# Optimization experiments

Measured on AMD Instinct MI355X. Metric: run time of the kernel, lower is better.

## Reference

```python
import jax, jax.numpy as jnp
import numpy as np
import math

B, H, D, P, N = 65536, 256, 32, 16, 32768
LOG_C = math.log(math.sqrt(2.0 * math.pi))


def setup_inputs() -> dict:
    key = jax.random.key(0)
    ks = jax.random.split(key, 8)
    h = jax.random.normal(ks[0], (B, H), dtype=jnp.float32)
    p = jax.random.normal(ks[1], (B, 2 * D), dtype=jnp.float32)
    X_obs = jax.random.normal(ks[2], (N, D), dtype=jnp.float32)
    M_obs = (jax.random.uniform(ks[3], (N, D)) < 0.5).astype(jnp.float32)
    i_obs = jnp.arange(N, dtype=jnp.int32)  # unique indices into batch rows
    std = math.sqrt(2.0 / (4 + P))
    w_prep = std * jax.random.normal(ks[4], (D, 4, P), dtype=jnp.float32)
    bias_prep = 0.1 * jnp.ones((D, P), dtype=jnp.float32)
    # keras GRUCell params (reset_after=True): kernel [in,3H], recurrent [H,3H], two biases [3H]
    gru_kernel = 0.05 * jax.random.normal(ks[5], (P * D, 3 * H), dtype=jnp.float32)
    gru_rec_kernel = 0.05 * jax.random.normal(ks[6], (H, 3 * H), dtype=jnp.float32)
    gru_bias_in = jnp.zeros((3 * H,), dtype=jnp.float32)
    gru_bias_rec = jnp.zeros((3 * H,), dtype=jnp.float32)
    return {"h": h, "p": p, "X_obs": X_obs, "M_obs": M_obs, "i_obs": i_obs,
            "w_prep": w_prep, "bias_prep": bias_prep,
            "gru_kernel": gru_kernel, "gru_rec_kernel": gru_rec_kernel,
            "gru_bias_in": gru_bias_in, "gru_bias_rec": gru_bias_rec}


def _gru_cell(x, h_prev, kernel, rec_kernel, bias_in, bias_rec):
    # keras GRUCell, reset_after=True, tanh / sigmoid activations
    mx = x @ kernel + bias_in            # [N, 3H]
    mh = h_prev @ rec_kernel + bias_rec  # [N, 3H]
    xz, xr, xh = jnp.split(mx, 3, axis=1)
    rz, rr, rh = jnp.split(mh, 3, axis=1)
    z = jax.nn.sigmoid(xz + rz)
    r = jax.nn.sigmoid(xr + rr)
    hh = jnp.tanh(xh + r * rh)
    return z * h_prev + (1.0 - z) * hh


def reference(h, p, X_obs, M_obs, i_obs, w_prep, bias_prep,
              gru_kernel, gru_rec_kernel, gru_bias_in, gru_bias_rec):
    d, ph = w_prep.shape[0], w_prep.shape[2]
    p_obs = p[i_obs]                      # gather [N, 2D]
    mean, logvar = jnp.split(p_obs, 2, axis=1)
    sigma = jnp.exp(0.5 * logvar)
    error = (X_obs - mean) / sigma
    losses = 0.5 * ((error * error + logvar + 2.0 * LOG_C) * M_obs)  # [N, D]
    gi = jnp.stack([X_obs, mean, logvar, error], axis=2)             # [N, D, 4]
    gi = jnp.einsum('ndk,dkp->ndp', gi, w_prep) + bias_prep          # per-feature matmul
    gi = jax.nn.relu(gi)
    gi = jnp.transpose(gi, (2, 0, 1))                                # [P, N, D]
    gi = (gi * M_obs).reshape(-1, ph * d)                            # [N, P*D] (TF reshape semantics)
    h_obs = h[i_obs]
    h_new = _gru_cell(gi, h_obs, gru_kernel, gru_rec_kernel, gru_bias_in, gru_bias_rec)
    h_out = h.at[i_obs].set(h_new)                                   # scatter-update
    return (h_out, losses)
```

## Files before the change

### kernel.cpp

```cpp
#include <hip/hip_runtime.h>
#include <hip/hip_bf16.h>
#include <math.h>

#define NROWS 32768
#define DD 32
#define PPH 16
#define HH 256
#define BB 65536
#define TWO_LOG_C 1.8378770664093453f

typedef __attribute__((ext_vector_type(8))) __bf16 bf16x8;
typedef __attribute__((ext_vector_type(4))) float f32x4;
typedef unsigned int u32;

__device__ __forceinline__ float sigm_f(float x) { return 1.0f / (1.0f + __expf(-x)); }
__device__ __forceinline__ float tanh_f(float x) { return 1.0f - 2.0f / (1.0f + __expf(2.0f * x)); }

__device__ __forceinline__ void gl_lds16(const __bf16* g, __bf16* l) {
    __builtin_amdgcn_global_load_lds(
        (const __attribute__((address_space(1))) u32*)g,
        (__attribute__((address_space(3))) u32*)l, 16, 0, 0);
}

__global__ __launch_bounds__(256) void prep_kernel(
    const float* __restrict__ p,
    const float* __restrict__ X_obs,
    const float* __restrict__ M_obs,
    const int*   __restrict__ i_obs,
    const float* __restrict__ w_prep,
    const float* __restrict__ bias_prep,
    float* __restrict__ losses_out,
    __bf16* __restrict__ G)
{
    __shared__ float w2[64][33];
    __shared__ float b2[16][33];
    int tid = threadIdx.x;
    for (int i = tid; i < 2048; i += 256) w2[i & 63][i >> 6] = w_prep[i];
    for (int i = tid; i < 512; i += 256)  b2[i & 15][i >> 4] = bias_prep[i];
    __syncthreads();

    int gid = blockIdx.x * 256 + tid;
    int n = gid >> 5;
    int d = gid & 31;
    int idx = i_obs[n];

    float mean   = p[idx * (2 * DD) + d];
    float logvar = p[idx * (2 * DD) + DD + d];
    float x      = X_obs[gid];
    float m      = M_obs[gid];

    float inv_sigma = __expf(-0.5f * logvar);
    float err = (x - mean) * inv_sigma;
    losses_out[gid] = 0.5f * ((err * err + logvar + TWO_LOG_C) * m);

    #pragma unroll
    for (int q = 0; q < PPH; ++q) {
        float v = x      * w2[q][d]
                + mean   * w2[16 + q][d]
                + logvar * w2[32 + q][d]
                + err    * w2[48 + q][d]
                + b2[q][d];
        v = fmaxf(v, 0.0f) * m;
        G[(size_t)q * (NROWS * DD) + gid] = (__bf16)v;
    }
}

__global__ __launch_bounds__(256) void mask_zero_kernel(u32* __restrict__ mask32) {
    mask32[blockIdx.x * 256 + threadIdx.x] = 0;
}
__global__ __launch_bounds__(256) void mask_set_kernel(
    const int* __restrict__ i_obs, unsigned char* __restrict__ mask) {
    mask[i_obs[blockIdx.x * 256 + threadIdx.x]] = 1;
}
__global__ __launch_bounds__(256) void copy_h_masked_kernel(
    const float4* __restrict__ h, const unsigned char* __restrict__ mask,
    float4* __restrict__ out, int n4)
{
    int i = blockIdx.x * 256 + threadIdx.x;
    int stride = gridDim.x * 256;
    for (; i < n4; i += stride) {
        int row = i >> 6;
        if (!mask[row]) out[i] = h[i];
    }
}

__global__ __launch_bounds__(256) void hgather_kernel(
    const float* __restrict__ h, const int* __restrict__ i_obs,
    __bf16* __restrict__ Hb)
{
    int gid = blockIdx.x * 256 + threadIdx.x;
    int n = gid >> 5, c = gid & 31;
    const float* src = h + (size_t)i_obs[n] * 256 + c * 8;
    float4 a = ((const float4*)src)[0];
    float4 b = ((const float4*)src)[1];
    bf16x8 v;
    v[0] = (__bf16)a.x; v[1] = (__bf16)a.y; v[2] = (__bf16)a.z; v[3] = (__bf16)a.w;
    v[4] = (__bf16)b.x; v[5] = (__bf16)b.y; v[6] = (__bf16)b.z; v[7] = (__bf16)b.w;
    *(bf16x8*)(Hb + (size_t)n * 256 + c * 8) = v;
}

__global__ __launch_bounds__(256) void transpose_w_kernel(
    const float* __restrict__ src, __bf16* __restrict__ dst, int K)
{
    __shared__ float t[64][65];
    int k0 = blockIdx.x * 64;
    int j0 = blockIdx.y * 64;
    int tx = threadIdx.x & 63, ty = threadIdx.x >> 6;
    #pragma unroll
    for (int i = 0; i < 16; ++i) {
        int k = ty * 16 + i;
        t[k][tx] = src[(size_t)(k0 + k) * 768 + j0 + tx];
    }
    __syncthreads();
    #pragma unroll
    for (int i = 0; i < 16; ++i) {
        int j = ty * 16 + i;
        dst[(size_t)(j0 + j) * K + k0 + tx] = (__bf16)t[tx][j];
    }
}

#define A_EL 4096
#define B_EL 6144

struct StageCtx {
    const __bf16 *G, *Hb, *Kt, *Rt;
    int i0, j0, wave, lane;
};

__device__ __forceinline__ void stage_step(int t, const StageCtx& c,
                                           __bf16* ldsA, __bf16* ldsB) {
    const bool ph1 = t < 16;
    const int k0 = (ph1 ? t : (t - 16)) * 32;
    const int Kd = ph1 ? 512 : 256;
    const __bf16* Asrc = ph1 ? c.G : c.Hb;
    const __bf16* Bsrc = ph1 ? c.Kt : c.Rt;
    __bf16* dA = ldsA + (t & 1) * A_EL;
    __bf16* dB = ldsB + (t & 1) * B_EL;
    #pragma unroll
    for (int s = 0; s < 5; ++s) {
        int u = c.wave * 5 + s;
        if (u < 8) {
            int sA = u * 64 + c.lane;
            int kg = sA >> 7, row = sA & 127;
            gl_lds16(Asrc + (size_t)(c.i0 + row) * Kd + k0 + kg * 8,
                     dA + u * 64 * 8);
        } else {
            int sB = (u - 8) * 64 + c.lane;
            int mat = sB >> 8, w = sB & 255;
            int bkg = w >> 6, bj = w & 63;
            gl_lds16(Bsrc + (size_t)(mat * 256 + c.j0 + bj) * Kd + k0 + bkg * 8,
                     dB + (u - 8) * 64 * 8);
        }
    }
}

__device__ __forceinline__ void compute_step(
    const __bf16* cA, const __bf16* cB,
    int kgrp, int lrow, int rw, int cw,
    f32x4 (&az)[4][2], f32x4 (&ar)[4][2], f32x4 (&ah)[4][2])
{
    bf16x8 af[4], bz[2], brf[2], bh[2];
    #pragma unroll
    for (int mt = 0; mt < 4; ++mt)
        af[mt] = *(const bf16x8*)(cA + (kgrp * 128 + rw * 64 + mt * 16 + lrow) * 8);
    #pragma unroll
    for (int jt = 0; jt < 2; ++jt) {
        int jj = cw * 32 + jt * 16 + lrow;
        bz[jt]  = *(const bf16x8*)(cB + (0 * 256 + kgrp * 64 + jj) * 8);
        brf[jt] = *(const bf16x8*)(cB + (1 * 256 + kgrp * 64 + jj) * 8);
        bh[jt]  = *(const bf16x8*)(cB + (2 * 256 + kgrp * 64 + jj) * 8);
    }
    #pragma unroll
    for (int mt = 0; mt < 4; ++mt)
        #pragma unroll
        for (int jt = 0; jt < 2; ++jt) {
            az[mt][jt] = __builtin_amdgcn_mfma_f32_16x16x32_bf16(af[mt], bz[jt],  az[mt][jt], 0, 0, 0);
            ar[mt][jt] = __builtin_amdgcn_mfma_f32_16x16x32_bf16(af[mt], brf[jt], ar[mt][jt], 0, 0, 0);
            ah[mt][jt] = __builtin_amdgcn_mfma_f32_16x16x32_bf16(af[mt], bh[jt],  ah[mt][jt], 0, 0, 0);
        }
}

__global__ __launch_bounds__(256, 2) void gru_mfma_kernel(
    const __bf16* __restrict__ G,
    const __bf16* __restrict__ Hb,
    const float*  __restrict__ h,
    const int*    __restrict__ i_obs,
    const __bf16* __restrict__ Kt,
    const __bf16* __restrict__ Rt,
    const float*  __restrict__ bi,
    const float*  __restrict__ brc,
    float* __restrict__ h_out)
{
    __shared__ __bf16 ldsA[2][A_EL];
    __shared__ __bf16 ldsB[2][B_EL];
    __shared__ int idx_s[128];

    const int tid  = threadIdx.x;
    const int lane = tid & 63;
    const int wave = tid >> 6;
    const int lrow = lane & 15;
    const int kgrp = lane >> 4;
    const int rw = wave >> 1;
    const int cw = wave & 1;

    int bid = blockIdx.x;
    int swz = (bid & 7) * 128 + (bid >> 3);
    const int i0 = (swz >> 2) * 128;
    const int j0 = (swz & 3) * 64;

    if (tid < 128) idx_s[tid] = i_obs[i0 + tid];

    f32x4 az[4][2], ar[4][2], axh[4][2], arh[4][2];
    const f32x4 zero4 = {0.f, 0.f, 0.f, 0.f};
    #pragma unroll
    for (int m = 0; m < 4; ++m)
        #pragma unroll
        for (int j = 0; j < 2; ++j) {
            az[m][j] = zero4; ar[m][j] = zero4; axh[m][j] = zero4; arh[m][j] = zero4;
        }

    StageCtx ctx{G, Hb, Kt, Rt, i0, j0, wave, lane};

    stage_step(0, ctx, &ldsA[0][0], &ldsB[0][0]);
    asm volatile("s_waitcnt vmcnt(0) lgkmcnt(0)" ::: "memory");
    __builtin_amdgcn_s_barrier();

    for (int t = 0; t < 16; ++t) {
        stage_step(t + 1, ctx, &ldsA[0][0], &ldsB[0][0]);
        compute_step(&ldsA[t & 1][0], &ldsB[t & 1][0], kgrp, lrow, rw, cw,
                     az, ar, axh);
        asm volatile("s_waitcnt vmcnt(0)" ::: "memory");
        __builtin_amdgcn_s_barrier();
    }
    for (int t = 16; t < 24; ++t) {
        if (t < 23) stage_step(t + 1, ctx, &ldsA[0][0], &ldsB[0][0]);
        compute_step(&ldsA[t & 1][0], &ldsB[t & 1][0], kgrp, lrow, rw, cw,
                     az, ar, arh);
        asm volatile("s_waitcnt vmcnt(0)" ::: "memory");
        __builtin_amdgcn_s_barrier();
    }

    #pragma unroll
    for (int mt = 0; mt < 4; ++mt) {
        int rl0 = rw * 64 + mt * 16 + kgrp * 4;
        #pragma unroll
        for (int jt = 0; jt < 2; ++jt) {
            int j = j0 + cw * 32 + jt * 16 + lrow;
            float b_z  = bi[j]       + brc[j];
            float b_r  = bi[256 + j] + brc[256 + j];
            float b_xh = bi[512 + j];
            float b_rh = brc[512 + j];
            #pragma unroll
            for (int r = 0; r < 4; ++r) {
                size_t hoff = (size_t)idx_s[rl0 + r] * 256 + j;
                float z  = sigm_f(az[mt][jt][r] + b_z);
                float rg = sigm_f(ar[mt][jt][r] + b_r);
                float hh = tanh_f(axh[mt][jt][r] + b_xh + rg * (arh[mt][jt][r] + b_rh));
                float hp = h[hoff];
                h_out[hoff] = z * hp + (1.0f - z) * hh;
            }
        }
    }
}

extern "C" void kernel_launch(void* const* d_in, const int* in_sizes, int n_in,
                              void* d_out, int out_size, void* d_ws, size_t ws_size,
                              hipStream_t stream) {
    const float* h         = (const float*)d_in[0];
    const float* p         = (const float*)d_in[1];
    const float* X_obs     = (const float*)d_in[2];
    const float* M_obs     = (const float*)d_in[3];
    const int*   i_obs     = (const int*)  d_in[4];
    const float* w_prep    = (const float*)d_in[5];
    const float* bias_prep = (const float*)d_in[6];
    const float* gk        = (const float*)d_in[7];
    const float* grk       = (const float*)d_in[8];
    const float* gbi       = (const float*)d_in[9];
    const float* gbr       = (const float*)d_in[10];

    float* out    = (float*)d_out;
    float* h_out  = out;
    float* losses = out + (size_t)BB * HH;

    char* ws = (char*)d_ws;
    __bf16* G    = (__bf16*)ws;
    __bf16* Kt   = (__bf16*)(ws + 33554432);
    __bf16* Rt   = (__bf16*)(ws + 34340864);
    __bf16* Hb   = (__bf16*)(ws + 34734080);
    unsigned char* mask = (unsigned char*)(ws + 51511296);

    mask_zero_kernel<<<64, 256, 0, stream>>>((u32*)mask);
    mask_set_kernel<<<NROWS / 256, 256, 0, stream>>>(i_obs, mask);
    transpose_w_kernel<<<dim3(8, 12), 256, 0, stream>>>(gk,  Kt, 512);
    transpose_w_kernel<<<dim3(4, 12), 256, 0, stream>>>(grk, Rt, 256);
    hgather_kernel<<<NROWS * 32 / 256, 256, 0, stream>>>(h, i_obs, Hb);
    prep_kernel<<<(NROWS * DD) / 256, 256, 0, stream>>>(
        p, X_obs, M_obs, i_obs, w_prep, bias_prep, losses, G);
    copy_h_masked_kernel<<<2048, 256, 0, stream>>>(
        (const float4*)h, mask, (float4*)h_out, BB * HH / 4);
    gru_mfma_kernel<<<1024, 256, 0, stream>>>(
        G, Hb, h, i_obs, Kt, Rt, gbi, gbr, h_out);
}
```

Baseline: 269.3 us.

## Fuse preprocessing kernels into one launch, swizzle LDS, deepen GEMM prefetch

Merges mask setup, weight transposes, h gathering, input prep and the h copy into a single pre_kernel launch. The h copy now writes every row unconditionally, and the GRU kernel later overwrites the observed rows, so the mask kernels go away. In the GEMM, LDS tiles switch to an XOR-swizzled row-major layout to cut bank conflicts, and the pipeline issues two stages ahead with partial vmcnt waits. The cost is extra write traffic for observed rows and more complex synchronization, which risks ordering hazards.

Result: faster. 218.5 us (-18.8%).

```diff
diff --git a/kernel.cpp b/kernel.cpp
--- a/kernel.cpp
+++ b/kernel.cpp
@@ -22,100 +22,92 @@
         (__attribute__((address_space(3))) u32*)l, 16, 0, 0);
 }
 
-__global__ __launch_bounds__(256) void prep_kernel(
+__global__ __launch_bounds__(256) void pre_kernel(
+    const float* __restrict__ h,
     const float* __restrict__ p,
     const float* __restrict__ X_obs,
     const float* __restrict__ M_obs,
     const int*   __restrict__ i_obs,
     const float* __restrict__ w_prep,
     const float* __restrict__ bias_prep,
-    float* __restrict__ losses_out,
-    __bf16* __restrict__ G)
+    const float* __restrict__ gk,
+    const float* __restrict__ grk,
+    float* __restrict__ losses,
+    __bf16* __restrict__ G,
+    __bf16* __restrict__ Hb,
+    __bf16* __restrict__ Kt,
+    __bf16* __restrict__ Rt,
+    float* __restrict__ h_out)
 {
-    __shared__ float w2[64][33];
-    __shared__ float b2[16][33];
-    int tid = threadIdx.x;
-    for (int i = tid; i < 2048; i += 256) w2[i & 63][i >> 6] = w_prep[i];
-    for (int i = tid; i < 512; i += 256)  b2[i & 15][i >> 4] = bias_prep[i];
-    __syncthreads();
-
-    int gid = blockIdx.x * 256 + tid;
-    int n = gid >> 5;
-    int d = gid & 31;
-    int idx = i_obs[n];
-
-    float mean   = p[idx * (2 * DD) + d];
-    float logvar = p[idx * (2 * DD) + DD + d];
-    float x      = X_obs[gid];
-    float m      = M_obs[gid];
-
-    float inv_sigma = __expf(-0.5f * logvar);
-    float err = (x - mean) * inv_sigma;
-    losses_out[gid] = 0.5f * ((err * err + logvar + TWO_LOG_C) * m);
-
-    #pragma unroll
-    for (int q = 0; q < PPH; ++q) {
-        float v = x      * w2[q][d]
-                + mean   * w2[16 + q][d]
-                + logvar * w2[32 + q][d]
-                + err    * w2[48 + q][d]
-                + b2[q][d];
-        v = fmaxf(v, 0.0f) * m;
-        G[(size_t)q * (NROWS * DD) + gid] = (__bf16)v;
-    }
-}
-
-__global__ __launch_bounds__(256) void mask_zero_kernel(u32* __restrict__ mask32) {
-    mask32[blockIdx.x * 256 + threadIdx.x] = 0;
-}
-__global__ __launch_bounds__(256) void mask_set_kernel(
-    const int* __restrict__ i_obs, unsigned char* __restrict__ mask) {
-    mask[i_obs[blockIdx.x * 256 + threadIdx.x]] = 1;
-}
-__global__ __launch_bounds__(256) void copy_h_masked_kernel(
-    const float4* __restrict__ h, const unsigned char* __restrict__ mask,
-    float4* __restrict__ out, int n4)
-{
-    int i = blockIdx.x * 256 + threadIdx.x;
-    int stride = gridDim.x * 256;
-    for (; i < n4; i += stride) {
-        int row = i >> 6;
-        if (!mask[row]) out[i] = h[i];
-    }
-}
-
-__global__ __launch_bounds__(256) void hgather_kernel(
-    const float* __restrict__ h, const int* __restrict__ i_obs,
-    __bf16* __restrict__ Hb)
-{
-    int gid = blockIdx.x * 256 + threadIdx.x;
-    int n = gid >> 5, c = gid & 31;
-    const float* src = h + (size_t)i_obs[n] * 256 + c * 8;
-    float4 a = ((const float4*)src)[0];
-    float4 b = ((const float4*)src)[1];
-    bf16x8 v;
-    v[0] = (__bf16)a.x; v[1] = (__bf16)a.y; v[2] = (__bf16)a.z; v[3] = (__bf16)a.w;
-    v[4] = (__bf16)b.x; v[5] = (__bf16)b.y; v[6] = (__bf16)b.z; v[7] = (__bf16)b.w;
-    *(bf16x8*)(Hb + (size_t)n * 256 + c * 8) = v;
-}
-
-__global__ __launch_bounds__(256) void transpose_w_kernel(
-    const float* __restrict__ src, __bf16* __restrict__ dst, int K)
-{
-    __shared__ float t[64][65];
-    int k0 = blockIdx.x * 64;
-    int j0 = blockIdx.y * 64;
-    int tx = threadIdx.x & 63, ty = threadIdx.x >> 6;
-    #pragma unroll
-    for (int i = 0; i < 16; ++i) {
-        int k = ty * 16 + i;
-        t[k][tx] = src[(size_t)(k0 + k) * 768 + j0 + tx];
-    }
-    __syncthreads();
-    #pragma unroll
-    for (int i = 0; i < 16; ++i) {
-        int j = ty * 16 + i;
-        dst[(size_t)(j0 + j) * K + k0 + tx] = (__bf16)t[tx][j];
+    __shared__ float arena[4160];
+    const int bid = blockIdx.x;
+    const int tid = threadIdx.x;
+
+    if (bid < 4096) {
+        float (*w2)[33] = (float(*)[33])arena;
+        float (*b2)[33] = (float(*)[33])(arena + 64 * 33);
+        for (int i = tid; i < 2048; i += 256) w2[i & 63][i >> 6] = w_prep[i];
+        for (int i = tid; i < 512; i += 256)  b2[i & 15][i >> 4] = bias_prep[i];
+        __syncthreads();
+
+        const int gid = bid * 256 + tid;
+        const int n = gid >> 5;
+        const int d = gid & 31;
+        const int idx = i_obs[n];
+
+        float mean   = p[idx * 64 + d];
+        float logvar = p[idx * 64 + 32 + d];
+        float x      = X_obs[gid];
+        float m      = M_obs[gid];
+
+        float inv_sigma = __expf(-0.5f * logvar);
+        float err = (x - mean) * inv_sigma;
+        losses[gid] = 0.5f * ((err * err + logvar + TWO_LOG_C) * m);
+
+        #pragma unroll
+        for (int q = 0; q < PPH; ++q) {
+            float v = x      * w2[q][d]
+                    + mean   * w2[16 + q][d]
+                    + logvar * w2[32 + q][d]
+                    + err    * w2[48 + q][d]
+                    + b2[q][d];
+            v = fmaxf(v, 0.0f) * m;
+            G[(size_t)q * (NROWS * DD) + gid] = (__bf16)v;
+        }
+
+        const float* hsrc = h + (size_t)idx * 256 + d * 8;
+        float4 a = ((const float4*)hsrc)[0];
+        float4 b = ((const float4*)hsrc)[1];
+        bf16x8 v8;
+        v8[0] = (__bf16)a.x; v8[1] = (__bf16)a.y; v8[2] = (__bf16)a.z; v8[3] = (__bf16)a.w;
+        v8[4] = (__bf16)b.x; v8[5] = (__bf16)b.y; v8[6] = (__bf16)b.z; v8[7] = (__bf16)b.w;
+        *(bf16x8*)(Hb + (size_t)n * 256 + d * 8) = v8;
+
+        const float4* hf4 = (const float4*)h;
+        float4* of4 = (float4*)h_out;
+        #pragma unroll
+        for (int k2 = 0; k2 < 4; ++k2) {
+            int i4 = gid + k2 * 1048576;
+            of4[i4] = hf4[i4];
+        }
+    } else {
+        float (*t)[65] = (float(*)[65])arena;
+        int b = bid - 4096;
+        const float* src; __bf16* dst; int K, k0, j0;
+        if (b < 96) { src = gk;  dst = Kt; K = 512; k0 = (b & 7) * 64; j0 = (b >> 3) * 64; }
+        else { b -= 96; src = grk; dst = Rt; K = 256; k0 = (b & 3) * 64; j0 = (b >> 2) * 64; }
+        int tx = tid & 63, ty = tid >> 6;
+        #pragma unroll
+        for (int i = 0; i < 16; ++i) {
+            int k = ty * 16 + i;
+            t[k][tx] = src[(size_t)(k0 + k) * 768 + j0 + tx];
+        }
+        __syncthreads();
+        #pragma unroll
+        for (int i = 0; i < 16; ++i) {
+            int j = ty * 16 + i;
+            dst[(size_t)(j0 + j) * K + k0 + tx] = (__bf16)t[tx][j];
+        }
     }
 }
 
@@ -136,20 +128,23 @@
     const __bf16* Bsrc = ph1 ? c.Kt : c.Rt;
     __bf16* dA = ldsA + (t & 1) * A_EL;
     __bf16* dB = ldsB + (t & 1) * B_EL;
+    const int rsub  = c.lane >> 2;
+    const int sslot = c.lane & 3;
     #pragma unroll
     for (int s = 0; s < 5; ++s) {
         int u = c.wave * 5 + s;
         if (u < 8) {
-            int sA = u * 64 + c.lane;
-            int kg = sA >> 7, row = sA & 127;
+            int row = u * 16 + rsub;
+            int kg = sslot ^ ((row >> 1) & 3);
             gl_lds16(Asrc + (size_t)(c.i0 + row) * Kd + k0 + kg * 8,
-                     dA + u * 64 * 8);
+                     dA + u * 512);
         } else {
-            int sB = (u - 8) * 64 + c.lane;
-            int mat = sB >> 8, w = sB & 255;
-            int bkg = w >> 6, bj = w & 63;
-            gl_lds16(Bsrc + (size_t)(mat * 256 + c.j0 + bj) * Kd + k0 + bkg * 8,
-                     dB + (u - 8) * 64 * 8);
+            int v = u - 8;
+            int br = v * 16 + rsub;
+            int kg = sslot ^ ((br >> 1) & 3);
+            int mat = br >> 6, jr = br & 63;
+            gl_lds16(Bsrc + (size_t)(mat * 256 + c.j0 + jr) * Kd + k0 + kg * 8,
+                     dB + v * 512);
         }
     }
 }
@@ -161,14 +156,17 @@
 {
     bf16x8 af[4], bz[2], brf[2], bh[2];
     #pragma unroll
-    for (int mt = 0; mt < 4; ++mt)
-        af[mt] = *(const bf16x8*)(cA + (kgrp * 128 + rw * 64 + mt * 16 + lrow) * 8);
+    for (int mt = 0; mt < 4; ++mt) {
+        int r = rw * 64 + mt * 16 + lrow;
+        af[mt] = *(const bf16x8*)(cA + r * 32 + (kgrp ^ ((r >> 1) & 3)) * 8);
+    }
     #pragma unroll
     for (int jt = 0; jt < 2; ++jt) {
         int jj = cw * 32 + jt * 16 + lrow;
-        bz[jt]  = *(const bf16x8*)(cB + (0 * 256 + kgrp * 64 + jj) * 8);
-        brf[jt] = *(const bf16x8*)(cB + (1 * 256 + kgrp * 64 + jj) * 8);
-        bh[jt]  = *(const bf16x8*)(cB + (2 * 256 + kgrp * 64 + jj) * 8);
+        int b0 = jj, b1 = 64 + jj, b2r = 128 + jj;
+        bz[jt]  = *(const bf16x8*)(cB + b0  * 32 + (kgrp ^ ((b0  >> 1) & 3)) * 8);
+        brf[jt] = *(const bf16x8*)(cB + b1  * 32 + (kgrp ^ ((b1  >> 1) & 3)) * 8);
+        bh[jt]  = *(const bf16x8*)(cB + b2r * 32 + (kgrp ^ ((b2r >> 1) & 3)) * 8);
     }
     #pragma unroll
     for (int mt = 0; mt < 4; ++mt)
@@ -209,6 +207,7 @@
     const int j0 = (swz & 3) * 64;
 
     if (tid < 128) idx_s[tid] = i_obs[i0 + tid];
+    asm volatile("s_waitcnt lgkmcnt(0)" ::: "memory");
 
     f32x4 az[4][2], ar[4][2], axh[4][2], arh[4][2];
     const f32x4 zero4 = {0.f, 0.f, 0.f, 0.f};
@@ -222,22 +221,26 @@
     StageCtx ctx{G, Hb, Kt, Rt, i0, j0, wave, lane};
 
     stage_step(0, ctx, &ldsA[0][0], &ldsB[0][0]);
-    asm volatile("s_waitcnt vmcnt(0) lgkmcnt(0)" ::: "memory");
-    __builtin_amdgcn_s_barrier();
-
+    stage_step(1, ctx, &ldsA[0][0], &ldsB[0][0]);
+
+    #pragma unroll
     for (int t = 0; t < 16; ++t) {
-        stage_step(t + 1, ctx, &ldsA[0][0], &ldsB[0][0]);
+        asm volatile("s_waitcnt vmcnt(5)" ::: "memory");
+        __builtin_amdgcn_s_barrier();
         compute_step(&ldsA[t & 1][0], &ldsB[t & 1][0], kgrp, lrow, rw, cw,
                      az, ar, axh);
-        asm volatile("s_waitcnt vmcnt(0)" ::: "memory");
         __builtin_amdgcn_s_barrier();
-    }
+        stage_step(t + 2, ctx, &ldsA[0][0], &ldsB[0][0]);
+    }
+    #pragma unroll
     for (int t = 16; t < 24; ++t) {
-        if (t < 23) stage_step(t + 1, ctx, &ldsA[0][0], &ldsB[0][0]);
+        if (t < 23) { asm volatile("s_waitcnt vmcnt(5)" ::: "memory"); }
+        else        { asm volatile("s_waitcnt vmcnt(0)" ::: "memory"); }
+        __builtin_amdgcn_s_barrier();
         compute_step(&ldsA[t & 1][0], &ldsB[t & 1][0], kgrp, lrow, rw, cw,
                      az, ar, arh);
-        asm volatile("s_waitcnt vmcnt(0)" ::: "memory");
         __builtin_amdgcn_s_barrier();
+        if (t + 2 < 24) stage_step(t + 2, ctx, &ldsA[0][0], &ldsB[0][0]);
     }
 
     #pragma unroll
@@ -283,21 +286,15 @@
     float* losses = out + (size_t)BB * HH;
 
     char* ws = (char*)d_ws;
-    __bf16* G    = (__bf16*)ws;
-    __bf16* Kt   = (__bf16*)(ws + 33554432);
-    __bf16* Rt   = (__bf16*)(ws + 34340864);
-    __bf16* Hb   = (__bf16*)(ws + 34734080);
-    unsigned char* mask = (unsigned char*)(ws + 51511296);
-
-    mask_zero_kernel<<<64, 256, 0, stream>>>((u32*)mask);
-    mask_set_kernel<<<NROWS / 256, 256, 0, stream>>>(i_obs, mask);
-    transpose_w_kernel<<<dim3(8, 12), 256, 0, stream>>>(gk,  Kt, 512);
-    transpose_w_kernel<<<dim3(4, 12), 256, 0, stream>>>(grk, Rt, 256);
-    hgather_kernel<<<NROWS * 32 / 256, 256, 0, stream>>>(h, i_obs, Hb);
-    prep_kernel<<<(NROWS * DD) / 256, 256, 0, stream>>>(
-        p, X_obs, M_obs, i_obs, w_prep, bias_prep, losses, G);
-    copy_h_masked_kernel<<<2048, 256, 0, stream>>>(
-        (const float4*)h, mask, (float4*)h_out, BB * HH / 4);
+    __bf16* G  = (__bf16*)ws;
+    __bf16* Kt = (__bf16*)(ws + 33554432);
+    __bf16* Rt = (__bf16*)(ws + 34340864);
+    __bf16* Hb = (__bf16*)(ws + 34734080);
+
+    pre_kernel<<<4240, 256, 0, stream>>>(
+        h, p, X_obs, M_obs, i_obs, w_prep, bias_prep, gk, grk,
+        losses, G, Hb, Kt, Rt, h_out);
+
     gru_mfma_kernel<<<1024, 256, 0, stream>>>(
         G, Hb, h, i_obs, Kt, Rt, gbi, gbr, h_out);
 }
```
